# Performance work log

Hardware: AMD Instinct MI355X
Metric: run time of the kernel (lower is better)

Reference implementation:

```python
import jax, jax.numpy as jnp
import numpy as np

T, B, E, H, L = 512, 64, 300, 800, 3  # seq, batch, embed, per-layer hidden, layers


def setup_inputs() -> dict:
    key = jax.random.key(0)
    ks = jax.random.split(key, 8)
    s = 0.05
    return {
        "sent": jax.random.normal(ks[0], (T, B, E), jnp.float32),
        "lengths": jax.random.randint(ks[1], (B,), 1, T + 1),
        "W0": jax.random.normal(ks[2], (E, 3 * H), jnp.float32) * s,
        "b0": jnp.zeros((3 * H,), jnp.float32),
        "W1": jax.random.normal(ks[3], (H, 3 * H), jnp.float32) * s,
        "b1": jnp.zeros((3 * H,), jnp.float32),
        "W2": jax.random.normal(ks[4], (H, 3 * H), jnp.float32) * s,
        "b2": jnp.zeros((3 * H,), jnp.float32),
    }


def _fo_pool(f, z):
    # c_t = f_t * z_t + (1 - f_t) * c_{t-1}, c_0 = 0  (ForgetMult)
    # linear recurrence c_t = a_t * c_{t-1} + b_t with a = 1-f, b = f*z
    a = 1.0 - f
    b = f * z
    def comb(c1, c2):
        a1, b1 = c1
        a2, b2 = c2
        return (a2 * a1, a2 * b1 + b2)
    _, C = jax.lax.associative_scan(comb, (a, b), axis=0)
    return C  # [T,B,H]; initial state is zero so C is exactly the pooled state


def _qrnn_layer(x, W, b):
    g = jnp.einsum('tbe,eh->tbh', x, W) + b  # [T,B,3H]
    z, f, o = jnp.split(g, 3, axis=-1)
    C = _fo_pool(jax.nn.sigmoid(f), jnp.tanh(z))
    return jax.nn.sigmoid(o) * C, C[-1]


def reference(sent, lengths, W0, b0, W1, b1, W2, b2):
    h = sent
    finals = []
    for W, bb in ((W0, b0), (W1, b1), (W2, b2)):
        h, c_last = _qrnn_layer(h, W, bb)
        finals.append(c_last)
    hn = jnp.stack(finals, axis=0)            # [L,B,H]
    out = jnp.transpose(hn, (1, 0, 2)).reshape(B, L * H)  # [B, L*H]
    return out
```

## Files before the change

kernel.cpp:

```cpp
#include <hip/hip_runtime.h>
#include <hip/hip_bf16.h>
#include <cstdint>
#include <cstddef>


typedef __bf16 bf16_t;
typedef __bf16 bf16x8 __attribute__((ext_vector_type(8)));
typedef float f32x4 __attribute__((ext_vector_type(4)));

#define T_C 128
#define NCHUNK 4
#define BATCH 64
#define EMB 300
#define HID 800
#define LDH 832
#define MC (T_C * BATCH)

__device__ __forceinline__ float fast_sigmoid(float x) {
  return 1.0f / (1.0f + __expf(-x));
}
__device__ __forceinline__ float fast_tanh(float x) {
  return 2.0f / (1.0f + __expf(-2.0f * x)) - 1.0f;
}
__device__ __forceinline__ float b2f(uint32_t u) {
  union { uint32_t i; float f; } x;
  x.i = u << 16;
  return x.f;
}

__global__ __launch_bounds__(256) void cast_reorder_a0(
    const float* __restrict__ X, bf16_t* __restrict__ Y) {
  int idx = blockIdx.x * 256 + threadIdx.x;
  if (idx >= 32768 * 320) return;
  int r = idx / 320, col = idx - r * 320;
  const int cc = r >> 13, b = (r >> 7) & 63, t = r & 127;
  const int src = (cc * 128 + t) * 64 + b;
  float v = (col < EMB) ? X[(size_t)src * EMB + col] : 0.0f;
  Y[idx] = (bf16_t)v;
}

__global__ __launch_bounds__(256) void transpose_cast_w(
    const float* __restrict__ W0, const float* __restrict__ W1,
    const float* __restrict__ W2, bf16_t* __restrict__ M0,
    bf16_t* __restrict__ M1, bf16_t* __restrict__ Z2) {
  const int z = blockIdx.z;
  const float* W = z == 0 ? W0 : (z == 1 ? W1 : W2);
  bf16_t* Wt = z == 0 ? M0 : (z == 1 ? M1 : Z2);
  const int K = z == 0 ? 300 : 800;
  const int Kpad = z == 0 ? 320 : 832;
  const int Npad = (z < 2) ? 2496 : 1664;
  const int i = blockIdx.x, j = blockIdx.y;
  if (i * 32 >= Npad || j * 32 >= Kpad) return;
  __shared__ float tile[32][33];
  const int tx = threadIdx.x & 31, ty = threadIdx.x >> 5;
#pragma unroll
  for (int r = 0; r < 32; r += 8) {
    const int k = j * 32 + ty + r;
    const int n = i * 32 + tx;
    int h, src;
    if (z < 2) {
      const int jt = n / 192, rr = n - jt * 192;
      if (rr < 128) {
        h = jt * 64 + (rr >> 1);
        src = (rr & 1) * 800 + h;
      } else {
        h = jt * 64 + (rr - 128);
        src = 1600 + h;
      }
    } else {
      h = n >> 1;
      src = (n & 1) * 800 + h;
    }
    const bool valid = (k < K) && (h < 800);
    tile[ty + r][tx] = valid ? W[(size_t)k * 2400 + src] : 0.0f;
  }
  __syncthreads();
#pragma unroll
  for (int r = 0; r < 32; r += 8) {
    const int n = i * 32 + ty + r, k = j * 32 + tx;
    if (n < Npad && k < Kpad)
      Wt[(size_t)n * Kpad + k] = (bf16_t)tile[tx][ty + r];
  }
}

__device__ __forceinline__ void stage16(const bf16_t* gp, bf16_t* lp) {
  __builtin_amdgcn_global_load_lds((__attribute__((address_space(1))) void*)gp,
                                   (__attribute__((address_space(3))) void*)lp,
                                   16, 0, 0);
}

template <int NTF, int ETS>
__device__ __forceinline__ void gemm_tile_to_lds(
    const bf16_t* __restrict__ A, const bf16_t* __restrict__ Bt,
    bf16_t* __restrict__ S, int K, int mBase, int nBase) {
  bf16_t* As = S;
  bf16_t* Bs = S + 8192;
  const int tid = threadIdx.x;
  const int wave = tid >> 6, lane = tid & 63;
  const int wm = wave >> 1, wn = wave & 1;
  const int srow = tid >> 3;
  const int scolSw = ((tid & 7) ^ (srow & 7)) * 8;
  const size_t aBase = (size_t)(mBase + srow) * K + scolSw;
  const size_t bBase = (size_t)(nBase + srow) * K + scolSw;
  const int ldsOff = tid * 8;

  f32x4 acc[4][NTF];
#pragma unroll
  for (int mt = 0; mt < 4; ++mt)
#pragma unroll
    for (int nt = 0; nt < NTF; ++nt) {
      f32x4 zz = {0.0f, 0.0f, 0.0f, 0.0f};
      acc[mt][nt] = zz;
    }

  const int fr = lane & 15, fq = lane >> 4;
  const int x0 = fr & 7;
  const int ckEl0 = (fq ^ x0) * 8;
  const int ckEl1 = ((4 + fq) ^ x0) * 8;

  for (int k0 = 0; k0 < K; k0 += 64) {
#pragma unroll
    for (int p = 0; p < 4; ++p)
      stage16(A + aBase + (size_t)(32 * p) * K + k0, &As[ldsOff + p * 2048]);
#pragma unroll
    for (int p = 0; p < NTF; ++p)
      stage16(Bt + bBase + (size_t)(32 * p) * K + k0, &Bs[ldsOff + p * 2048]);
    __syncthreads();
#pragma unroll
    for (int kh = 0; kh < 2; ++kh) {
      const int ck = kh ? ckEl1 : ckEl0;
      bf16x8 af[4], bfv[NTF];
#pragma unroll
      for (int mt = 0; mt < 4; ++mt)
        af[mt] = *(const bf16x8*)&As[(wm * 64 + mt * 16 + fr) * 64 + ck];
#pragma unroll
      for (int nt = 0; nt < NTF; ++nt)
        bfv[nt] = *(const bf16x8*)&Bs[(wn * (16 * NTF) + nt * 16 + fr) * 64 + ck];
#pragma unroll
      for (int mt = 0; mt < 4; ++mt)
#pragma unroll
        for (int nt = 0; nt < NTF; ++nt)
          acc[mt][nt] = __builtin_amdgcn_mfma_f32_16x16x32_bf16(
              af[mt], bfv[nt], acc[mt][nt], 0, 0, 0);
    }
    __syncthreads();
  }
  bf16_t* Et = S;
#pragma unroll
  for (int mt = 0; mt < 4; ++mt)
#pragma unroll
    for (int nt = 0; nt < NTF; ++nt)
#pragma unroll
      for (int r = 0; r < 4; ++r)
        Et[(wm * 64 + mt * 16 + fq * 4 + r) * ETS + wn * (16 * NTF) + nt * 16 +
           fr] = (bf16_t)acc[mt][nt][r];
  __syncthreads();
}

__global__ __launch_bounds__(256, 3) void gemm_scan_h(
    const bf16_t* __restrict__ A, const bf16_t* __restrict__ Wm,
    const float* __restrict__ bias, bf16_t* __restrict__ Hout,
    float* __restrict__ carry, float* __restrict__ outC, int K, int outOff,
    int first, int last) {
  __shared__ __align__(16) bf16_t S[25088];
  __shared__ float SA[4][64], SB[4][64], SC[4][64];
  const int nT = gridDim.x;
  const int L = blockIdx.y * nT + blockIdx.x;
  const int xcd = L & 7, j = L >> 3;
  const int b = xcd * 8 + j / nT;
  const int ntile = j % nT;
  gemm_tile_to_lds<6, 196>(A, Wm, S, K, b * 128, ntile * 192);

  const uint32_t* Ep = (const uint32_t*)S;
  const int tid = threadIdx.x;
  const int hl = tid & 63, s = tid >> 6;
  const int h = ntile * 64 + hl;
  const bool hOK = (h < HID);
  const int hb = hOK ? h : 0;
  const float bz = bias[hb], bf = bias[hb + 800], bo = bias[hb + 1600];

  float av[32], bv[32];
  float Aa = 1.0f, Bb = 0.0f;
#pragma unroll
  for (int q = 0; q < 32; ++q) {
    const int t = s * 32 + q;
    const uint32_t v = Ep[t * 98 + hl];
    const float zv = fast_tanh(b2f(v & 0xffffu) + bz);
    const float fv = fast_sigmoid(b2f(v >> 16) + bf);
    av[q] = 1.0f - fv;
    bv[q] = fv * zv;
    Aa *= av[q];
    Bb = fmaf(av[q], Bb, bv[q]);
  }
  SA[s][hl] = Aa;
  SB[s][hl] = Bb;
  __syncthreads();
  if (tid < 64) {
    const int h2 = ntile * 64 + tid;
    const bool ok2 = (h2 < HID);
    float c = (first || !ok2) ? 0.0f : carry[b * HID + h2];
#pragma unroll
    for (int ss = 0; ss < 4; ++ss) {
      SC[ss][tid] = c;
      c = fmaf(SA[ss][tid], c, SB[ss][tid]);
    }
    if (ok2) {
      carry[b * HID + h2] = c;
      if (last) outC[b * 2400 + outOff + h2] = c;
    }
  }
  __syncthreads();
  float c = SC[s][hl];
#pragma unroll
  for (int q = 0; q < 32; ++q) {
    const int t = s * 32 + q;
    c = fmaf(av[q], c, bv[q]);
    const float o = fast_sigmoid((float)S[t * 196 + 128 + hl] + bo);
    Hout[(size_t)(b * 128 + t) * LDH + h] =
        hOK ? (bf16_t)(o * c) : (bf16_t)0.0f;
  }
}

__global__ __launch_bounds__(256, 3) void gemm_scan_c(
    const bf16_t* __restrict__ A, const bf16_t* __restrict__ Wzf,
    const float* __restrict__ bias, float* __restrict__ carry,
    float* __restrict__ outC, int K, int outOff, int first, int last) {
  __shared__ __align__(16) bf16_t S[17920];
  __shared__ float SA[4][64], SB[4][64];
  const int nT = gridDim.x;
  const int L = blockIdx.y * nT + blockIdx.x;
  const int xcd = L & 7, j = L >> 3;
  const int b = xcd * 8 + j / nT;
  const int ntile = j % nT;
  gemm_tile_to_lds<4, 140>(A, Wzf, S, K, b * 128, ntile * 128);

  const uint32_t* Ep = (const uint32_t*)S;
  const int tid = threadIdx.x;
  const int hl = tid & 63, s = tid >> 6;
  const int h = ntile * 64 + hl;
  const bool hOK = (h < HID);
  const int hb = hOK ? h : 0;
  const float bz = bias[hb], bf = bias[hb + 800];

  float Aa = 1.0f, Bb = 0.0f;
#pragma unroll
  for (int q = 0; q < 32; ++q) {
    const int t = s * 32 + q;
    const uint32_t v = Ep[t * 70 + hl];
    const float zv = fast_tanh(b2f(v & 0xffffu) + bz);
    const float fv = fast_sigmoid(b2f(v >> 16) + bf);
    const float a = 1.0f - fv;
    Aa *= a;
    Bb = fmaf(a, Bb, fv * zv);
  }
  SA[s][hl] = Aa;
  SB[s][hl] = Bb;
  __syncthreads();
  if (tid < 64) {
    const int h2 = ntile * 64 + tid;
    const bool ok2 = (h2 < HID);
    float c = (first || !ok2) ? 0.0f : carry[b * HID + h2];
#pragma unroll
    for (int ss = 0; ss < 4; ++ss) c = fmaf(SA[ss][tid], c, SB[ss][tid]);
    if (ok2) {
      carry[b * HID + h2] = c;
      if (last) outC[b * 2400 + outOff + h2] = c;
    }
  }
}

extern "C" void kernel_launch(void* const* d_in, const int* in_sizes, int n_in,
                              void* d_out, int out_size, void* d_ws, size_t ws_size,
                              hipStream_t stream) {
  const float* sent = (const float*)d_in[0];
  const float* W0 = (const float*)d_in[2];
  const float* b0 = (const float*)d_in[3];
  const float* W1 = (const float*)d_in[4];
  const float* b1 = (const float*)d_in[5];
  const float* W2 = (const float*)d_in[6];
  const float* b2 = (const float*)d_in[7];
  float* out = (float*)d_out;

  char* ws = (char*)d_ws;
  size_t off = 0;
  auto alloc = [&](size_t bytes) {
    void* p = ws + off;
    off += (bytes + 255) & ~(size_t)255;
    return p;
  };
  bf16_t* Wm0 = (bf16_t*)alloc((size_t)2496 * 320 * 2);
  bf16_t* Wm1 = (bf16_t*)alloc((size_t)2496 * 832 * 2);
  bf16_t* Wzf2 = (bf16_t*)alloc((size_t)1664 * 832 * 2);
  bf16_t* A0 = (bf16_t*)alloc((size_t)32768 * 320 * 2);
  bf16_t* H0c = (bf16_t*)alloc((size_t)MC * LDH * 2);
  bf16_t* H1c = (bf16_t*)alloc((size_t)MC * LDH * 2);
  float* car0 = (float*)alloc((size_t)BATCH * HID * 4);
  float* car1 = (float*)alloc((size_t)BATCH * HID * 4);
  float* car2 = (float*)alloc((size_t)BATCH * HID * 4);
  if (off > ws_size) return;

  cast_reorder_a0<<<(32768 * 320 + 255) / 256, 256, 0, stream>>>(sent, A0);
  transpose_cast_w<<<dim3(78, 26, 3), 256, 0, stream>>>(W0, W1, W2, Wm0, Wm1,
                                                        Wzf2);

  for (int c = 0; c < NCHUNK; ++c) {
    const int first = (c == 0), last = (c == NCHUNK - 1);
    const bf16_t* A0c = A0 + (size_t)c * MC * 320;
    gemm_scan_h<<<dim3(13, 64), 256, 0, stream>>>(A0c, Wm0, b0, H0c, car0, out,
                                                  320, 0, first, last);
    gemm_scan_h<<<dim3(13, 64), 256, 0, stream>>>(H0c, Wm1, b1, H1c, car1, out,
                                                  832, 800, first, last);
    gemm_scan_c<<<dim3(13, 64), 256, 0, stream>>>(H1c, Wzf2, b2, car2, out,
                                                  832, 1600, first, last);
  }
}
```

Measured before the change: 575.3 us.

## Process full sequence per block with in-LDS carry instead of chunked launches

```diff
diff --git a/kernel.cpp b/kernel.cpp
--- a/kernel.cpp
+++ b/kernel.cpp
@@ -8,13 +8,11 @@
 typedef __bf16 bf16x8 __attribute__((ext_vector_type(8)));
 typedef float f32x4 __attribute__((ext_vector_type(4)));
 
-#define T_C 128
-#define NCHUNK 4
+#define T_SEQ 512
 #define BATCH 64
 #define EMB 300
 #define HID 800
 #define LDH 832
-#define MC (T_C * BATCH)
 
 __device__ __forceinline__ float fast_sigmoid(float x) {
   return 1.0f / (1.0f + __expf(-x));
@@ -33,8 +31,8 @@
   int idx = blockIdx.x * 256 + threadIdx.x;
   if (idx >= 32768 * 320) return;
   int r = idx / 320, col = idx - r * 320;
-  const int cc = r >> 13, b = (r >> 7) & 63, t = r & 127;
-  const int src = (cc * 128 + t) * 64 + b;
+  const int b = r >> 9, t = r & 511;
+  const int src = t * 64 + b;
   float v = (col < EMB) ? X[(size_t)src * EMB + col] : 0.0f;
   Y[idx] = (bf16_t)v;
 }
@@ -160,18 +158,15 @@
 __global__ __launch_bounds__(256, 3) void gemm_scan_h(
     const bf16_t* __restrict__ A, const bf16_t* __restrict__ Wm,
     const float* __restrict__ bias, bf16_t* __restrict__ Hout,
-    float* __restrict__ carry, float* __restrict__ outC, int K, int outOff,
-    int first, int last) {
+    float* __restrict__ outC, int K, int outOff) {
   __shared__ __align__(16) bf16_t S[25088];
-  __shared__ float SA[4][64], SB[4][64], SC[4][64];
+  __shared__ float SA[4][64], SB[4][64], SC[4][64], Ccar[64];
   const int nT = gridDim.x;
   const int L = blockIdx.y * nT + blockIdx.x;
   const int xcd = L & 7, j = L >> 3;
   const int b = xcd * 8 + j / nT;
   const int ntile = j % nT;
-  gemm_tile_to_lds<6, 196>(A, Wm, S, K, b * 128, ntile * 192);
-
-  const uint32_t* Ep = (const uint32_t*)S;
+
   const int tid = threadIdx.x;
   const int hl = tid & 63, s = tid >> 6;
   const int h = ntile * 64 + hl;
@@ -179,93 +174,100 @@
   const int hb = hOK ? h : 0;
   const float bz = bias[hb], bf = bias[hb + 800], bo = bias[hb + 1600];
 
-  float av[32], bv[32];
-  float Aa = 1.0f, Bb = 0.0f;
-#pragma unroll
-  for (int q = 0; q < 32; ++q) {
-    const int t = s * 32 + q;
-    const uint32_t v = Ep[t * 98 + hl];
-    const float zv = fast_tanh(b2f(v & 0xffffu) + bz);
-    const float fv = fast_sigmoid(b2f(v >> 16) + bf);
-    av[q] = 1.0f - fv;
-    bv[q] = fv * zv;
-    Aa *= av[q];
-    Bb = fmaf(av[q], Bb, bv[q]);
-  }
-  SA[s][hl] = Aa;
-  SB[s][hl] = Bb;
-  __syncthreads();
-  if (tid < 64) {
-    const int h2 = ntile * 64 + tid;
-    const bool ok2 = (h2 < HID);
-    float c = (first || !ok2) ? 0.0f : carry[b * HID + h2];
-#pragma unroll
-    for (int ss = 0; ss < 4; ++ss) {
-      SC[ss][tid] = c;
-      c = fmaf(SA[ss][tid], c, SB[ss][tid]);
-    }
-    if (ok2) {
-      carry[b * HID + h2] = c;
-      if (last) outC[b * 2400 + outOff + h2] = c;
-    }
-  }
-  __syncthreads();
-  float c = SC[s][hl];
-#pragma unroll
-  for (int q = 0; q < 32; ++q) {
-    const int t = s * 32 + q;
-    c = fmaf(av[q], c, bv[q]);
-    const float o = fast_sigmoid((float)S[t * 196 + 128 + hl] + bo);
-    Hout[(size_t)(b * 128 + t) * LDH + h] =
-        hOK ? (bf16_t)(o * c) : (bf16_t)0.0f;
+  for (int sub = 0; sub < 4; ++sub) {
+    gemm_tile_to_lds<6, 196>(A, Wm, S, K, b * T_SEQ + sub * 128, ntile * 192);
+
+    const uint32_t* Ep = (const uint32_t*)S;
+    float av[32], bv[32];
+    float Aa = 1.0f, Bb = 0.0f;
+#pragma unroll
+    for (int q = 0; q < 32; ++q) {
+      const int t = s * 32 + q;
+      const uint32_t v = Ep[t * 98 + hl];
+      const float zv = fast_tanh(b2f(v & 0xffffu) + bz);
+      const float fv = fast_sigmoid(b2f(v >> 16) + bf);
+      av[q] = 1.0f - fv;
+      bv[q] = fv * zv;
+      Aa *= av[q];
+      Bb = fmaf(av[q], Bb, bv[q]);
+    }
+    SA[s][hl] = Aa;
+    SB[s][hl] = Bb;
+    __syncthreads();
+    if (tid < 64) {
+      float c = (sub == 0) ? 0.0f : Ccar[tid];
+#pragma unroll
+      for (int ss = 0; ss < 4; ++ss) {
+        SC[ss][tid] = c;
+        c = fmaf(SA[ss][tid], c, SB[ss][tid]);
+      }
+      Ccar[tid] = c;
+      if (sub == 3) {
+        const int h2 = ntile * 64 + tid;
+        if (h2 < HID) outC[b * 2400 + outOff + h2] = c;
+      }
+    }
+    __syncthreads();
+    float c = SC[s][hl];
+#pragma unroll
+    for (int q = 0; q < 32; ++q) {
+      const int t = s * 32 + q;
+      c = fmaf(av[q], c, bv[q]);
+      const float o = fast_sigmoid((float)S[t * 196 + 128 + hl] + bo);
+      Hout[(size_t)(b * T_SEQ + sub * 128 + t) * LDH + h] =
+          hOK ? (bf16_t)(o * c) : (bf16_t)0.0f;
+    }
+    __syncthreads();
   }
 }
 
 __global__ __launch_bounds__(256, 3) void gemm_scan_c(
     const bf16_t* __restrict__ A, const bf16_t* __restrict__ Wzf,
-    const float* __restrict__ bias, float* __restrict__ carry,
-    float* __restrict__ outC, int K, int outOff, int first, int last) {
+    const float* __restrict__ bias, float* __restrict__ outC, int K,
+    int outOff) {
   __shared__ __align__(16) bf16_t S[17920];
-  __shared__ float SA[4][64], SB[4][64];
+  __shared__ float SA[4][64], SB[4][64], Ccar[64];
   const int nT = gridDim.x;
   const int L = blockIdx.y * nT + blockIdx.x;
   const int xcd = L & 7, j = L >> 3;
   const int b = xcd * 8 + j / nT;
   const int ntile = j % nT;
-  gemm_tile_to_lds<4, 140>(A, Wzf, S, K, b * 128, ntile * 128);
-
-  const uint32_t* Ep = (const uint32_t*)S;
+
   const int tid = threadIdx.x;
   const int hl = tid & 63, s = tid >> 6;
   const int h = ntile * 64 + hl;
-  const bool hOK = (h < HID);
-  const int hb = hOK ? h : 0;
+  const int hb = (h < HID) ? h : 0;
   const float bz = bias[hb], bf = bias[hb + 800];
 
-  float Aa = 1.0f, Bb = 0.0f;
-#pragma unroll
-  for (int q = 0; q < 32; ++q) {
-    const int t = s * 32 + q;
-    const uint32_t v = Ep[t * 70 + hl];
-    const float zv = fast_tanh(b2f(v & 0xffffu) + bz);
-    const float fv = fast_sigmoid(b2f(v >> 16) + bf);
-    const float a = 1.0f - fv;
-    Aa *= a;
-    Bb = fmaf(a, Bb, fv * zv);
-  }
-  SA[s][hl] = Aa;
-  SB[s][hl] = Bb;
-  __syncthreads();
-  if (tid < 64) {
-    const int h2 = ntile * 64 + tid;
-    const bool ok2 = (h2 < HID);
-    float c = (first || !ok2) ? 0.0f : carry[b * HID + h2];
-#pragma unroll
-    for (int ss = 0; ss < 4; ++ss) c = fmaf(SA[ss][tid], c, SB[ss][tid]);
-    if (ok2) {
-      carry[b * HID + h2] = c;
-      if (last) outC[b * 2400 + outOff + h2] = c;
-    }
+  for (int sub = 0; sub < 4; ++sub) {
+    gemm_tile_to_lds<4, 140>(A, Wzf, S, K, b * T_SEQ + sub * 128, ntile * 128);
+
+    const uint32_t* Ep = (const uint32_t*)S;
+    float Aa = 1.0f, Bb = 0.0f;
+#pragma unroll
+    for (int q = 0; q < 32; ++q) {
+      const int t = s * 32 + q;
+      const uint32_t v = Ep[t * 70 + hl];
+      const float zv = fast_tanh(b2f(v & 0xffffu) + bz);
+      const float fv = fast_sigmoid(b2f(v >> 16) + bf);
+      const float a = 1.0f - fv;
+      Aa *= a;
+      Bb = fmaf(a, Bb, fv * zv);
+    }
+    SA[s][hl] = Aa;
+    SB[s][hl] = Bb;
+    __syncthreads();
+    if (tid < 64) {
+      float c = (sub == 0) ? 0.0f : Ccar[tid];
+#pragma unroll
+      for (int ss = 0; ss < 4; ++ss) c = fmaf(SA[ss][tid], c, SB[ss][tid]);
+      Ccar[tid] = c;
+      if (sub == 3) {
+        const int h2 = ntile * 64 + tid;
+        if (h2 < HID) outC[b * 2400 + outOff + h2] = c;
+      }
+    }
+    __syncthreads();
   }
 }
 
@@ -292,25 +294,15 @@
   bf16_t* Wm1 = (bf16_t*)alloc((size_t)2496 * 832 * 2);
   bf16_t* Wzf2 = (bf16_t*)alloc((size_t)1664 * 832 * 2);
   bf16_t* A0 = (bf16_t*)alloc((size_t)32768 * 320 * 2);
-  bf16_t* H0c = (bf16_t*)alloc((size_t)MC * LDH * 2);
-  bf16_t* H1c = (bf16_t*)alloc((size_t)MC * LDH * 2);
-  float* car0 = (float*)alloc((size_t)BATCH * HID * 4);
-  float* car1 = (float*)alloc((size_t)BATCH * HID * 4);
-  float* car2 = (float*)alloc((size_t)BATCH * HID * 4);
+  bf16_t* H0 = (bf16_t*)alloc((size_t)32768 * LDH * 2);
+  bf16_t* H1 = (bf16_t*)alloc((size_t)32768 * LDH * 2);
   if (off > ws_size) return;
 
   cast_reorder_a0<<<(32768 * 320 + 255) / 256, 256, 0, stream>>>(sent, A0);
   transpose_cast_w<<<dim3(78, 26, 3), 256, 0, stream>>>(W0, W1, W2, Wm0, Wm1,
                                                         Wzf2);
 
-  for (int c = 0; c < NCHUNK; ++c) {
-    const int first = (c == 0), last = (c == NCHUNK - 1);
-    const bf16_t* A0c = A0 + (size_t)c * MC * 320;
-    gemm_scan_h<<<dim3(13, 64), 256, 0, stream>>>(A0c, Wm0, b0, H0c, car0, out,
-                                                  320, 0, first, last);
-    gemm_scan_h<<<dim3(13, 64), 256, 0, stream>>>(H0c, Wm1, b1, H1c, car1, out,
-                                                  832, 800, first, last);
-    gemm_scan_c<<<dim3(13, 64), 256, 0, stream>>>(H1c, Wzf2, b2, car2, out,
-                                                  832, 1600, first, last);
-  }
-}
+  gemm_scan_h<<<dim3(13, 64), 256, 0, stream>>>(A0, Wm0, b0, H0, out, 320, 0);
+  gemm_scan_h<<<dim3(13, 64), 256, 0, stream>>>(H0, Wm1, b1, H1, out, 832, 800);
+  gemm_scan_c<<<dim3(13, 64), 256, 0, stream>>>(H1, Wzf2, b2, out, 832, 1600);
+}
```

Result: slower. 607.3 us (+5.6%).

## Overlap layer-2 scan of chunk c with layer-0 GEMM of next chunk

Applied to the files above, without the earlier changes.

```diff
diff --git a/kernel.cpp b/kernel.cpp
--- a/kernel.cpp
+++ b/kernel.cpp
@@ -157,18 +157,12 @@
   __syncthreads();
 }
 
-__global__ __launch_bounds__(256, 3) void gemm_scan_h(
+__device__ __forceinline__ void scan_h_body(
     const bf16_t* __restrict__ A, const bf16_t* __restrict__ Wm,
     const float* __restrict__ bias, bf16_t* __restrict__ Hout,
     float* __restrict__ carry, float* __restrict__ outC, int K, int outOff,
-    int first, int last) {
-  __shared__ __align__(16) bf16_t S[25088];
-  __shared__ float SA[4][64], SB[4][64], SC[4][64];
-  const int nT = gridDim.x;
-  const int L = blockIdx.y * nT + blockIdx.x;
-  const int xcd = L & 7, j = L >> 3;
-  const int b = xcd * 8 + j / nT;
-  const int ntile = j % nT;
+    int first, int last, int b, int ntile, bf16_t* S, float (*SA)[64],
+    float (*SB)[64], float (*SC)[64]) {
   gemm_tile_to_lds<6, 196>(A, Wm, S, K, b * 128, ntile * 192);
 
   const uint32_t* Ep = (const uint32_t*)S;
@@ -221,25 +215,18 @@
   }
 }
 
-__global__ __launch_bounds__(256, 3) void gemm_scan_c(
+__device__ __forceinline__ void scan_c_body(
     const bf16_t* __restrict__ A, const bf16_t* __restrict__ Wzf,
     const float* __restrict__ bias, float* __restrict__ carry,
-    float* __restrict__ outC, int K, int outOff, int first, int last) {
-  __shared__ __align__(16) bf16_t S[17920];
-  __shared__ float SA[4][64], SB[4][64];
-  const int nT = gridDim.x;
-  const int L = blockIdx.y * nT + blockIdx.x;
-  const int xcd = L & 7, j = L >> 3;
-  const int b = xcd * 8 + j / nT;
-  const int ntile = j % nT;
+    float* __restrict__ outC, int K, int outOff, int first, int last, int b,
+    int ntile, bf16_t* S, float (*SA)[64], float (*SB)[64]) {
   gemm_tile_to_lds<4, 140>(A, Wzf, S, K, b * 128, ntile * 128);
 
   const uint32_t* Ep = (const uint32_t*)S;
   const int tid = threadIdx.x;
   const int hl = tid & 63, s = tid >> 6;
   const int h = ntile * 64 + hl;
-  const bool hOK = (h < HID);
-  const int hb = hOK ? h : 0;
+  const int hb = (h < HID) ? h : 0;
   const float bz = bias[hb], bf = bias[hb + 800];
 
   float Aa = 1.0f, Bb = 0.0f;
@@ -266,6 +253,58 @@
       carry[b * HID + h2] = c;
       if (last) outC[b * 2400 + outOff + h2] = c;
     }
+  }
+}
+
+__device__ __forceinline__ void block_tile(int& b, int& ntile) {
+  const int nT = 13;
+  const int L = blockIdx.y * nT + blockIdx.x;
+  const int xcd = L & 7, j = L >> 3;
+  b = xcd * 8 + j / nT;
+  ntile = j % nT;
+}
+
+__global__ __launch_bounds__(256, 3) void gemm_scan_h(
+    const bf16_t* __restrict__ A, const bf16_t* __restrict__ Wm,
+    const float* __restrict__ bias, bf16_t* __restrict__ Hout,
+    float* __restrict__ carry, float* __restrict__ outC, int K, int outOff,
+    int first, int last) {
+  __shared__ __align__(16) bf16_t S[25088];
+  __shared__ float SA[4][64], SB[4][64], SC[4][64];
+  int b, ntile;
+  block_tile(b, ntile);
+  scan_h_body(A, Wm, bias, Hout, carry, outC, K, outOff, first, last, b,
+              ntile, S, SA, SB, SC);
+}
+
+__global__ __launch_bounds__(256, 4) void gemm_scan_c(
+    const bf16_t* __restrict__ A, const bf16_t* __restrict__ Wzf,
+    const float* __restrict__ bias, float* __restrict__ carry,
+    float* __restrict__ outC, int K, int outOff, int first, int last) {
+  __shared__ __align__(16) bf16_t S[17920];
+  __shared__ float SA[4][64], SB[4][64];
+  int b, ntile;
+  block_tile(b, ntile);
+  scan_c_body(A, Wzf, bias, carry, outC, K, outOff, first, last, b, ntile, S,
+              SA, SB);
+}
+
+__global__ __launch_bounds__(256, 3) void gemm_scan_mix(
+    const bf16_t* __restrict__ H1c, const bf16_t* __restrict__ Wzf2,
+    const float* __restrict__ b2, float* __restrict__ car2, int firstC2,
+    const bf16_t* __restrict__ A0n, const bf16_t* __restrict__ Wm0,
+    const float* __restrict__ b0, bf16_t* __restrict__ H0c,
+    float* __restrict__ car0, int lastC0, float* __restrict__ outC) {
+  __shared__ __align__(16) bf16_t S[25088];
+  __shared__ float SA[4][64], SB[4][64], SC[4][64];
+  int b, ntile;
+  block_tile(b, ntile);
+  if (blockIdx.z == 0) {
+    scan_c_body(H1c, Wzf2, b2, car2, outC, 832, 1600, firstC2, 0, b, ntile, S,
+                SA, SB);
+  } else {
+    scan_h_body(A0n, Wm0, b0, H0c, car0, outC, 320, 0, 0, lastC0, b, ntile, S,
+                SA, SB, SC);
   }
 }
 
@@ -303,14 +342,20 @@
   transpose_cast_w<<<dim3(78, 26, 3), 256, 0, stream>>>(W0, W1, W2, Wm0, Wm1,
                                                         Wzf2);
 
+  gemm_scan_h<<<dim3(13, 64), 256, 0, stream>>>(A0, Wm0, b0, H0c, car0, out,
+                                                320, 0, 1, 0);
   for (int c = 0; c < NCHUNK; ++c) {
     const int first = (c == 0), last = (c == NCHUNK - 1);
-    const bf16_t* A0c = A0 + (size_t)c * MC * 320;
-    gemm_scan_h<<<dim3(13, 64), 256, 0, stream>>>(A0c, Wm0, b0, H0c, car0, out,
-                                                  320, 0, first, last);
     gemm_scan_h<<<dim3(13, 64), 256, 0, stream>>>(H0c, Wm1, b1, H1c, car1, out,
                                                   832, 800, first, last);
-    gemm_scan_c<<<dim3(13, 64), 256, 0, stream>>>(H1c, Wzf2, b2, car2, out,
-                                                  832, 1600, first, last);
-  }
-}
+    if (c < NCHUNK - 1) {
+      const bf16_t* A0n = A0 + (size_t)(c + 1) * MC * 320;
+      gemm_scan_mix<<<dim3(13, 64, 2), 256, 0, stream>>>(
+          H1c, Wzf2, b2, car2, first, A0n, Wm0, b0, H0c, car0,
+          (c + 1 == NCHUNK - 1) ? 1 : 0, out);
+    } else {
+      gemm_scan_c<<<dim3(13, 64), 256, 0, stream>>>(H1c, Wzf2, b2, car2, out,
+                                                    832, 1600, 0, 1);
+    }
+  }
+}
```

Result: faster. 553.0 us (-3.9%).

## Pipeline QRNN layers across time chunks in merged multi-role launches

Applied to the files above, without the earlier changes.

```diff
diff --git a/kernel.cpp b/kernel.cpp
--- a/kernel.cpp
+++ b/kernel.cpp
@@ -157,18 +157,12 @@
   __syncthreads();
 }
 
-__global__ __launch_bounds__(256, 3) void gemm_scan_h(
+__device__ __forceinline__ void scan_h_body(
     const bf16_t* __restrict__ A, const bf16_t* __restrict__ Wm,
     const float* __restrict__ bias, bf16_t* __restrict__ Hout,
     float* __restrict__ carry, float* __restrict__ outC, int K, int outOff,
-    int first, int last) {
-  __shared__ __align__(16) bf16_t S[25088];
-  __shared__ float SA[4][64], SB[4][64], SC[4][64];
-  const int nT = gridDim.x;
-  const int L = blockIdx.y * nT + blockIdx.x;
-  const int xcd = L & 7, j = L >> 3;
-  const int b = xcd * 8 + j / nT;
-  const int ntile = j % nT;
+    int first, int last, int b, int ntile, bf16_t* S, float (*SA)[64],
+    float (*SB)[64], float (*SC)[64]) {
   gemm_tile_to_lds<6, 196>(A, Wm, S, K, b * 128, ntile * 192);
 
   const uint32_t* Ep = (const uint32_t*)S;
@@ -221,25 +215,18 @@
   }
 }
 
-__global__ __launch_bounds__(256, 3) void gemm_scan_c(
+__device__ __forceinline__ void scan_c_body(
     const bf16_t* __restrict__ A, const bf16_t* __restrict__ Wzf,
     const float* __restrict__ bias, float* __restrict__ carry,
-    float* __restrict__ outC, int K, int outOff, int first, int last) {
-  __shared__ __align__(16) bf16_t S[17920];
-  __shared__ float SA[4][64], SB[4][64];
-  const int nT = gridDim.x;
-  const int L = blockIdx.y * nT + blockIdx.x;
-  const int xcd = L & 7, j = L >> 3;
-  const int b = xcd * 8 + j / nT;
-  const int ntile = j % nT;
+    float* __restrict__ outC, int K, int outOff, int first, int last, int b,
+    int ntile, bf16_t* S, float (*SA)[64], float (*SB)[64]) {
   gemm_tile_to_lds<4, 140>(A, Wzf, S, K, b * 128, ntile * 128);
 
   const uint32_t* Ep = (const uint32_t*)S;
   const int tid = threadIdx.x;
   const int hl = tid & 63, s = tid >> 6;
   const int h = ntile * 64 + hl;
-  const bool hOK = (h < HID);
-  const int hb = hOK ? h : 0;
+  const int hb = (h < HID) ? h : 0;
   const float bz = bias[hb], bf = bias[hb + 800];
 
   float Aa = 1.0f, Bb = 0.0f;
@@ -267,6 +254,42 @@
       if (last) outC[b * 2400 + outOff + h2] = c;
     }
   }
+}
+
+__device__ __forceinline__ void block_tile(int& b, int& ntile) {
+  const int nT = 13;
+  const int L = blockIdx.y * nT + blockIdx.x;
+  const int xcd = L & 7, j = L >> 3;
+  b = xcd * 8 + j / nT;
+  ntile = j % nT;
+}
+
+struct Role {
+  const bf16_t* A;
+  const bf16_t* W;
+  const float* bias;
+  bf16_t* Hout;
+  float* carry;
+  int K;
+  int outOff;
+  int type;
+  int first;
+  int last;
+};
+
+__global__ __launch_bounds__(256, 3) void gemm_scan_multi(
+    Role r0, Role r1, Role r2, float* __restrict__ outC) {
+  __shared__ __align__(16) bf16_t S[25088];
+  __shared__ float SA[4][64], SB[4][64], SC[4][64];
+  int b, ntile;
+  block_tile(b, ntile);
+  const Role r = blockIdx.z == 0 ? r0 : (blockIdx.z == 1 ? r1 : r2);
+  if (r.type == 1)
+    scan_h_body(r.A, r.W, r.bias, r.Hout, r.carry, outC, r.K, r.outOff,
+                r.first, r.last, b, ntile, S, SA, SB, SC);
+  else
+    scan_c_body(r.A, r.W, r.bias, r.carry, outC, r.K, r.outOff, r.first,
+                r.last, b, ntile, S, SA, SB);
 }
 
 extern "C" void kernel_launch(void* const* d_in, const int* in_sizes, int n_in,
@@ -292,8 +315,11 @@
   bf16_t* Wm1 = (bf16_t*)alloc((size_t)2496 * 832 * 2);
   bf16_t* Wzf2 = (bf16_t*)alloc((size_t)1664 * 832 * 2);
   bf16_t* A0 = (bf16_t*)alloc((size_t)32768 * 320 * 2);
-  bf16_t* H0c = (bf16_t*)alloc((size_t)MC * LDH * 2);
-  bf16_t* H1c = (bf16_t*)alloc((size_t)MC * LDH * 2);
+  bf16_t* H0buf[2], *H1buf[2];
+  H0buf[0] = (bf16_t*)alloc((size_t)MC * LDH * 2);
+  H0buf[1] = (bf16_t*)alloc((size_t)MC * LDH * 2);
+  H1buf[0] = (bf16_t*)alloc((size_t)MC * LDH * 2);
+  H1buf[1] = (bf16_t*)alloc((size_t)MC * LDH * 2);
   float* car0 = (float*)alloc((size_t)BATCH * HID * 4);
   float* car1 = (float*)alloc((size_t)BATCH * HID * 4);
   float* car2 = (float*)alloc((size_t)BATCH * HID * 4);
@@ -303,14 +329,37 @@
   transpose_cast_w<<<dim3(78, 26, 3), 256, 0, stream>>>(W0, W1, W2, Wm0, Wm1,
                                                         Wzf2);
 
-  for (int c = 0; c < NCHUNK; ++c) {
-    const int first = (c == 0), last = (c == NCHUNK - 1);
-    const bf16_t* A0c = A0 + (size_t)c * MC * 320;
-    gemm_scan_h<<<dim3(13, 64), 256, 0, stream>>>(A0c, Wm0, b0, H0c, car0, out,
-                                                  320, 0, first, last);
-    gemm_scan_h<<<dim3(13, 64), 256, 0, stream>>>(H0c, Wm1, b1, H1c, car1, out,
-                                                  832, 800, first, last);
-    gemm_scan_c<<<dim3(13, 64), 256, 0, stream>>>(H1c, Wzf2, b2, car2, out,
-                                                  832, 1600, first, last);
-  }
-}
+  auto mkL0 = [&](int c) -> Role {
+    return Role{A0 + (size_t)c * MC * 320, Wm0, b0, H0buf[c & 1], car0,
+                320, 0, 1, c == 0, c == NCHUNK - 1};
+  };
+  auto mkL1 = [&](int c) -> Role {
+    return Role{H0buf[c & 1], Wm1, b1, H1buf[c & 1], car1,
+                832, 800, 1, c == 0, c == NCHUNK - 1};
+  };
+  auto mkL2 = [&](int c) -> Role {
+    return Role{H1buf[c & 1], Wzf2, b2, nullptr, car2,
+                832, 1600, 2, c == 0, c == NCHUNK - 1};
+  };
+
+  {
+    Role a = mkL0(0);
+    gemm_scan_multi<<<dim3(13, 64, 1), 256, 0, stream>>>(a, a, a, out);
+  }
+  {
+    Role a = mkL1(0), b_ = mkL0(1);
+    gemm_scan_multi<<<dim3(13, 64, 2), 256, 0, stream>>>(a, b_, b_, out);
+  }
+  for (int c = 1; c <= 2; ++c) {
+    Role a = mkL1(c), b_ = mkL2(c - 1), d = mkL0(c + 1);
+    gemm_scan_multi<<<dim3(13, 64, 3), 256, 0, stream>>>(a, b_, d, out);
+  }
+  {
+    Role a = mkL1(3), b_ = mkL2(2);
+    gemm_scan_multi<<<dim3(13, 64, 2), 256, 0, stream>>>(a, b_, b_, out);
+  }
+  {
+    Role a = mkL2(3);
+    gemm_scan_multi<<<dim3(13, 64, 1), 256, 0, stream>>>(a, a, a, out);
+  }
+}
```

After: 495.8 us. 13.8% less time.
